# Kernel tuning notes

Measured on AMD Instinct MI355X. Metric: run time of the kernel, lower is better.

## Reference

```python
import jax, jax.numpy as jnp
import numpy as np

B, LAT, MEM, IMG = 8192, 256, 200, 128
THRESHOLD = 1.0 / MEM          # sparse-addressing threshold 1/MEM_DIM
EPS_SHRINK = 1e-12             # module epsilon
EPS_COS = 1e-8                 # torch CosineSimilarity default eps
EPS_L1 = 1e-12                 # torch F.normalize default eps


def setup_inputs() -> dict:
    key = jax.random.key(0)
    k1, k2, k3 = jax.random.split(key, 3)
    z = jax.random.normal(k1, (B, LAT), dtype=jnp.float32)          # encoder latent
    memory = jax.random.normal(k2, (MEM, LAT), dtype=jnp.float32) * 0.05  # kaiming-scale memory
    W = jax.random.normal(k3, (IMG * IMG, LAT), dtype=jnp.float32) * 0.02  # linear weight
    b = jnp.zeros((IMG * IMG,), dtype=jnp.float32)
    return {"z": z, "memory": memory, "W": W, "b": b}


def reference(z, memory, W, b):
    # Cosine similarity via normalized matmul (no [B,MEM,LAT] repeat tensors)
    zn = jnp.linalg.norm(z, axis=1, keepdims=True)          # [B,1]
    mn = jnp.linalg.norm(memory, axis=1, keepdims=True)     # [MEM,1]
    logits = (z @ memory.T) / jnp.maximum(zn * mn.T, EPS_COS)  # [B,MEM]
    w = jax.nn.softmax(logits, axis=1)
    # sparse shrinkage: relu(w-t)*w/(|w-t|+eps)
    w = jax.nn.relu(w - THRESHOLD) * w / (jnp.abs(w - THRESHOLD) + EPS_SHRINK)
    # L1 normalize over memory dim
    w = w / jnp.maximum(jnp.sum(jnp.abs(w), axis=1, keepdims=True), EPS_L1)
    z_hat = w @ memory                                      # [B,LAT]
    x_hat = (z_hat @ W.T + b).reshape(-1, 1, IMG, IMG)      # [B,1,128,128]
    return x_hat, z_hat, w
```

## Files before the change

### kernel.cpp

```cpp
#include <hip/hip_runtime.h>
#include <hip/hip_bf16.h>
#include <stdint.h>

#define B_DIM   8192
#define LAT     256
#define MEM_DIM 200
#define MEM_PAD 208
#define NPIX    16384
#define RPB     16
#define CHUNK   25

typedef short bf16x8 __attribute__((ext_vector_type(8)));
typedef float f32x4  __attribute__((ext_vector_type(4)));

__device__ __forceinline__ float wred_sum(float v) {
#pragma unroll
  for (int m = 32; m; m >>= 1) v += __shfl_xor(v, m, 64);
  return v;
}
__device__ __forceinline__ float wred_max(float v) {
#pragma unroll
  for (int m = 32; m; m >>= 1) v = fmaxf(v, __shfl_xor(v, m, 64));
  return v;
}
__device__ __forceinline__ unsigned short f2bf(float f) {
  unsigned u = __builtin_bit_cast(unsigned, f);
  u = u + 0x7FFFu + ((u >> 16) & 1u);
  return (unsigned short)(u >> 16);
}
__device__ __forceinline__ float bf2f(unsigned short h) {
  return __builtin_bit_cast(float, (unsigned)h << 16);
}
__device__ __forceinline__ void split3(float v, unsigned short& h, unsigned short& m,
                                       unsigned short& l) {
  h = f2bf(v);
  float r1 = v - bf2f(h);
  m = f2bf(r1);
  float r2 = r1 - bf2f(m);
  l = f2bf(r2);
}

__global__ void __launch_bounds__(64) mem_norm_kernel(const float* __restrict__ mem,
                                                      float* __restrict__ mn,
                                                      unsigned short* __restrict__ mem_h,
                                                      unsigned short* __restrict__ mem_m,
                                                      unsigned short* __restrict__ mem_l) {
  const int m = blockIdx.x, lane = threadIdx.x;
  if (m >= MEM_DIM) {
    ushort4 zz = {0, 0, 0, 0};
    ((ushort4*)(mem_h + (size_t)m * LAT))[lane] = zz;
    ((ushort4*)(mem_m + (size_t)m * LAT))[lane] = zz;
    ((ushort4*)(mem_l + (size_t)m * LAT))[lane] = zz;
    return;
  }
  float4 v = ((const float4*)(mem + (size_t)m * LAT))[lane];
  ushort4 h, md, l;
  split3(v.x, h.x, md.x, l.x); split3(v.y, h.y, md.y, l.y);
  split3(v.z, h.z, md.z, l.z); split3(v.w, h.w, md.w, l.w);
  ((ushort4*)(mem_h + (size_t)m * LAT))[lane] = h;
  ((ushort4*)(mem_m + (size_t)m * LAT))[lane] = md;
  ((ushort4*)(mem_l + (size_t)m * LAT))[lane] = l;
  float ss = v.x * v.x + v.y * v.y + v.z * v.z + v.w * v.w;
  ss = wred_sum(ss);
  if (lane == 0) mn[m] = sqrtf(ss);
}

__global__ void __launch_bounds__(256) zsplit_kernel(const float* __restrict__ z,
                                                     unsigned short* __restrict__ z_h,
                                                     unsigned short* __restrict__ z_m,
                                                     unsigned short* __restrict__ z_l) {
  const int i = blockIdx.x * 256 + threadIdx.x;
  float4 v = ((const float4*)z)[i];
  ushort4 h, md, l;
  split3(v.x, h.x, md.x, l.x); split3(v.y, h.y, md.y, l.y);
  split3(v.z, h.z, md.z, l.z); split3(v.w, h.w, md.w, l.w);
  ((ushort4*)z_h)[i] = h;
  ((ushort4*)z_m)[i] = md;
  ((ushort4*)z_l)[i] = l;
}

__global__ void __launch_bounds__(256) convert_w_kernel(const float* __restrict__ W,
                                                        unsigned short* __restrict__ Wb) {
  const int i = blockIdx.x * 256 + threadIdx.x;
  float4 v = ((const float4*)W)[i];
  ushort4 o;
  o.x = f2bf(v.x); o.y = f2bf(v.y); o.z = f2bf(v.z); o.w = f2bf(v.w);
  ((ushort4*)Wb)[i] = o;
}

__global__ void __launch_bounds__(256) row_kernel(
    const float* __restrict__ z, const float* __restrict__ mem,
    const float* __restrict__ mn_g,
    const unsigned short* __restrict__ z_h, const unsigned short* __restrict__ z_m,
    const unsigned short* __restrict__ z_l,
    const unsigned short* __restrict__ mem_h, const unsigned short* __restrict__ mem_m,
    const unsigned short* __restrict__ mem_l,
    float* __restrict__ zhat_out, float* __restrict__ w_out,
    unsigned short* __restrict__ zhat_bf) {
  __shared__ float msh[CHUNK * LAT];
  __shared__ float lw[RPB][MEM_DIM];
  __shared__ float mnsh[MEM_DIM];

  const int tid = threadIdx.x;
  const int lane = tid & 63;
  const int wid = tid >> 6;
  const int row0 = blockIdx.x * RPB;

  if (tid < MEM_DIM) mnsh[tid] = mn_g[tid];

  float4 zr[4];
  float zn[4];
#pragma unroll
  for (int r = 0; r < 4; ++r) {
    const int row = row0 + wid * 4 + r;
    zr[r] = *(const float4*)(z + (size_t)row * LAT + lane * 4);
    float ss = zr[r].x * zr[r].x + zr[r].y * zr[r].y + zr[r].z * zr[r].z + zr[r].w * zr[r].w;
    zn[r] = sqrtf(wred_sum(ss));
  }

  {
    const int fr_ = lane & 15;
    const int kq8 = (lane >> 4) * 8;
    const size_t zoff = (size_t)(row0 + fr_) * LAT + kq8;
    const unsigned short* zh_p = z_h + zoff;
    const unsigned short* zm_p = z_m + zoff;
    const unsigned short* zl_p = z_l + zoff;
    for (int nf = wid; nf <= 12; nf += 4) {
      const size_t moff = (size_t)(nf * 16 + fr_) * LAT + kq8;
      const unsigned short* mh_p = mem_h + moff;
      const unsigned short* mm_p = mem_m + moff;
      const unsigned short* ml_p = mem_l + moff;
      f32x4 a = {};
#pragma unroll
      for (int kk = 0; kk < 8; ++kk) {
        bf16x8 zh = *(const bf16x8*)(zh_p + kk * 32);
        bf16x8 zm = *(const bf16x8*)(zm_p + kk * 32);
        bf16x8 zl = *(const bf16x8*)(zl_p + kk * 32);
        bf16x8 mh = *(const bf16x8*)(mh_p + kk * 32);
        bf16x8 mm = *(const bf16x8*)(mm_p + kk * 32);
        bf16x8 ml = *(const bf16x8*)(ml_p + kk * 32);
        a = __builtin_amdgcn_mfma_f32_16x16x32_bf16(zm, mm, a, 0, 0, 0);
        a = __builtin_amdgcn_mfma_f32_16x16x32_bf16(zh, ml, a, 0, 0, 0);
        a = __builtin_amdgcn_mfma_f32_16x16x32_bf16(zl, mh, a, 0, 0, 0);
        a = __builtin_amdgcn_mfma_f32_16x16x32_bf16(zm, mh, a, 0, 0, 0);
        a = __builtin_amdgcn_mfma_f32_16x16x32_bf16(zh, mm, a, 0, 0, 0);
        a = __builtin_amdgcn_mfma_f32_16x16x32_bf16(zh, mh, a, 0, 0, 0);
      }
      const int m = nf * 16 + fr_;
      if (m < MEM_DIM) {
#pragma unroll
        for (int q = 0; q < 4; ++q)
          lw[(lane >> 4) * 4 + q][m] = a[q];
      }
    }
  }
  __syncthreads();

  const float t = 0.005f;
#pragma unroll
  for (int r = 0; r < 4; ++r) {
    const int lr = wid * 4 + r;
    float lg[4];
#pragma unroll
    for (int i = 0; i < 4; ++i) {
      const int m = lane + 64 * i;
      lg[i] = (m < MEM_DIM) ? lw[lr][m] / fmaxf(zn[r] * mnsh[m], 1e-8f) : -1e30f;
    }
    float mx = wred_max(fmaxf(fmaxf(lg[0], lg[1]), fmaxf(lg[2], lg[3])));
    float e[4]; float s = 0.f;
#pragma unroll
    for (int i = 0; i < 4; ++i) {
      const int m = lane + 64 * i;
      e[i] = (m < MEM_DIM) ? expf(lg[i] - mx) : 0.f;
      s += e[i];
    }
    s = wred_sum(s);
    float sv[4]; float l1 = 0.f;
#pragma unroll
    for (int i = 0; i < 4; ++i) {
      const float wv = e[i] / s;
      const float d = wv - t;
      sv[i] = fmaxf(d, 0.f) * wv / (fabsf(d) + 1e-12f);
      l1 += sv[i];
    }
    l1 = wred_sum(l1);
    const float dnm = fmaxf(l1, 1e-12f);
#pragma unroll
    for (int i = 0; i < 4; ++i) {
      const int m = lane + 64 * i;
      if (m < MEM_DIM) {
        const float wn = sv[i] / dnm;
        lw[lr][m] = wn;
        w_out[(size_t)(row0 + lr) * MEM_DIM + m] = wn;
      }
    }
  }

  f32x4 acc[4] = {};
  for (int c = 0; c < 8; ++c) {
    __syncthreads();
    const float4* gsrc = (const float4*)(mem + (size_t)c * CHUNK * LAT);
    float4* msh4 = (float4*)msh;
    for (int i = tid; i < CHUNK * 64; i += 256) msh4[i] = gsrc[i];
    __syncthreads();
    for (int mm = 0; mm < CHUNK; ++mm) {
      float4 mv = ((float4*)msh)[mm * 64 + lane];
      const int m = c * CHUNK + mm;
#pragma unroll
      for (int r = 0; r < 4; ++r) {
        const float wm = lw[wid * 4 + r][m];
        acc[r][0] += wm * mv.x; acc[r][1] += wm * mv.y;
        acc[r][2] += wm * mv.z; acc[r][3] += wm * mv.w;
      }
    }
  }
#pragma unroll
  for (int r = 0; r < 4; ++r) {
    const int row = row0 + wid * 4 + r;
    float4 o; o.x = acc[r][0]; o.y = acc[r][1]; o.z = acc[r][2]; o.w = acc[r][3];
    *(float4*)(zhat_out + (size_t)row * LAT + lane * 4) = o;
    ushort4 ob; ob.x = f2bf(o.x); ob.y = f2bf(o.y); ob.z = f2bf(o.z); ob.w = f2bf(o.w);
    *(ushort4*)(zhat_bf + (size_t)row * LAT + lane * 4) = ob;
  }
}

#define STAGE(bufbase, t)                                                      \
  {                                                                            \
    const int k0_ = (t) * 32;                                                  \
    _Pragma("unroll")                                                          \
    for (int cc = 0; cc < 2; ++cc) {                                           \
      const int r_ = r0 + cc * 16;                                             \
      __builtin_amdgcn_global_load_lds(                                        \
          (const __attribute__((address_space(1))) void*)(const void*)         \
              (A + (size_t)(brow + r_) * LAT + k0_ + kq),                      \
          (__attribute__((address_space(3))) void*)(void*)                     \
              &smem[(bufbase) + (ch0 + cc) * 1024], 16, 0, 0);                 \
      __builtin_amdgcn_global_load_lds(                                        \
          (const __attribute__((address_space(1))) void*)(const void*)         \
              (Bw + (size_t)(bcol + r_) * LAT + k0_ + kq),                     \
          (__attribute__((address_space(3))) void*)(void*)                     \
              &smem[(bufbase) + 8192 + (ch0 + cc) * 1024], 16, 0, 0);          \
    }                                                                          \
  }

#define GEMM_PROLOG_AND_KLOOP                                                  \
  const int tid = threadIdx.x;                                                 \
  const int lane = tid & 63;                                                   \
  const int wid = tid >> 6;                                                    \
  const int swz = (blockIdx.x & 7) * 1024 + (blockIdx.x >> 3);                 \
  const int st = swz >> 8;                                                     \
  const int loc = swz & 255;                                                   \
  const int tm = (st >> 3) * 16 + (loc & 15);                                  \
  const int tn = (st & 7) * 16 + (loc >> 4);                                   \
  const int brow = tm * 128;                                                   \
  const int bcol = tn * 128;                                                   \
  const int wr = wid >> 1, wc = wid & 1;                                       \
  const int ch0 = wid * 2;                                                     \
  const int r0 = ch0 * 16 + (lane >> 2);                                       \
  const int kq = (lane & 3) * 8;                                               \
  f32x4 acc[4][4] = {};                                                        \
  STAGE(0, 0);                                                                 \
  STAGE(16384, 1);                                                             \
  STAGE(32768, 2);                                                             \
  _Pragma("unroll")                                                            \
  for (int t = 0; t < 8; ++t) {                                                \
    if (t < 6)       asm volatile("s_waitcnt vmcnt(8)" ::: "memory");          \
    else if (t == 6) asm volatile("s_waitcnt vmcnt(4)" ::: "memory");          \
    else             asm volatile("s_waitcnt vmcnt(0)" ::: "memory");          \
    __builtin_amdgcn_sched_barrier(0);                                         \
    __builtin_amdgcn_s_barrier();                                              \
    const int bufb = (t % 3) * 16384;                                          \
    bf16x8 af[4], bfr[4];                                                      \
    _Pragma("unroll")                                                          \
    for (int mf = 0; mf < 4; ++mf)                                             \
      af[mf] = *(const bf16x8*)&smem[bufb + (wr * 64 + mf * 16 + (lane & 15)) * 64 + (lane >> 4) * 16]; \
    _Pragma("unroll")                                                          \
    for (int nf = 0; nf < 4; ++nf)                                             \
      bfr[nf] = *(const bf16x8*)&smem[bufb + 8192 + (wc * 64 + nf * 16 + (lane & 15)) * 64 + (lane >> 4) * 16]; \
    asm volatile("s_waitcnt lgkmcnt(0)" ::: "memory");                         \
    __builtin_amdgcn_sched_barrier(0);                                         \
    __builtin_amdgcn_s_barrier();                                              \
    if (t + 3 < 8) STAGE(((t + 3) % 3) * 16384, t + 3);                        \
    _Pragma("unroll")                                                          \
    for (int mf = 0; mf < 4; ++mf)                                             \
      _Pragma("unroll")                                                        \
      for (int nf = 0; nf < 4; ++nf)                                           \
        acc[mf][nf] = __builtin_amdgcn_mfma_f32_16x16x32_bf16(af[mf], bfr[nf], acc[mf][nf], 0, 0, 0); \
  }

#define TSTRIDE 68
__global__ void __launch_bounds__(256, 3) gemm_xhat_kernel(
    const unsigned short* __restrict__ A, const unsigned short* __restrict__ Bw,
    const float* __restrict__ bias, float* __restrict__ C) {
  __shared__ __align__(16) unsigned char smem[49152];

  if (blockIdx.x < 768) {
    const int d = blockIdx.x >> 8;
    for (int i = 0; i < d; ++i) {
#pragma unroll
      for (int s = 0; s < 8; ++s)
        __builtin_amdgcn_s_sleep(100);
    }
  }

  GEMM_PROLOG_AND_KLOOP

  __syncthreads();
  float* tt = (float*)(smem + wid * (16 * TSTRIDE * 4));

  const int colq = (lane & 15) * 4;
  const int col0 = bcol + wc * 64 + colq;
  const float4 bv4 = *(const float4*)(bias + col0);

#pragma unroll
  for (int mf = 0; mf < 4; ++mf) {
#pragma unroll
    for (int nf = 0; nf < 4; ++nf) {
      const int cl = nf * 16 + (lane & 15);
#pragma unroll
      for (int q = 0; q < 4; ++q)
        tt[((lane >> 4) * 4 + q) * TSTRIDE + cl] = acc[mf][nf][q];
    }
#pragma unroll
    for (int rr = 0; rr < 4; ++rr) {
      const int rl = rr * 4 + (lane >> 4);
      float4 v = *(const float4*)&tt[rl * TSTRIDE + colq];
      f32x4 ve;
      ve[0] = v.x + bv4.x; ve[1] = v.y + bv4.y;
      ve[2] = v.z + bv4.z; ve[3] = v.w + bv4.w;
      const int row = brow + wr * 64 + mf * 16 + rl;
      __builtin_nontemporal_store(ve, (f32x4*)&C[(size_t)row * NPIX + col0]);
    }
  }
}

extern "C" void kernel_launch(void* const* d_in, const int* in_sizes, int n_in,
                              void* d_out, int out_size, void* d_ws, size_t ws_size,
                              hipStream_t stream) {
  const float* z    = (const float*)d_in[0];
  const float* mem  = (const float*)d_in[1];
  const float* W    = (const float*)d_in[2];
  const float* bias = (const float*)d_in[3];

  float* xhat = (float*)d_out;
  float* zhat = xhat + (size_t)B_DIM * NPIX;
  float* wout = zhat + (size_t)B_DIM * LAT;

  unsigned short* z_h   = (unsigned short*)xhat;
  unsigned short* z_m   = z_h + (size_t)B_DIM * LAT;
  unsigned short* z_l   = z_m + (size_t)B_DIM * LAT;
  unsigned short* mem_h = z_l + (size_t)B_DIM * LAT;
  unsigned short* mem_m = mem_h + (size_t)MEM_PAD * LAT;
  unsigned short* mem_l = mem_m + (size_t)MEM_PAD * LAT;

  unsigned short* Wb  = (unsigned short*)d_ws;
  unsigned short* zhb = Wb + (size_t)NPIX * LAT;
  float* mn = (float*)(zhb + (size_t)B_DIM * LAT);

  mem_norm_kernel<<<MEM_PAD, 64, 0, stream>>>(mem, mn, mem_h, mem_m, mem_l);
  zsplit_kernel<<<(B_DIM * LAT / 4) / 256, 256, 0, stream>>>(z, z_h, z_m, z_l);
  convert_w_kernel<<<(NPIX * LAT / 4) / 256, 256, 0, stream>>>(W, Wb);
  row_kernel<<<B_DIM / RPB, 256, 0, stream>>>(z, mem, mn, z_h, z_m, z_l,
                                              mem_h, mem_m, mem_l, zhat, wout, zhb);
  gemm_xhat_kernel<<<8192, 256, 0, stream>>>(zhb, Wb, bias, xhat);
}
```

Baseline: 222.7 us.

## Compute z_hat = w @ memory with split-bf16 MFMA using transposed memory

Replaces the scalar FP32 w@memory loop in row_kernel, which staged memory chunks in LDS, with 3-way bf16-split MFMA products. The memory matrix is pre-transposed and split into high, mid and low bf16 parts in mem_norm_kernel. The weights are split into LDS per block. This aims to move the second small GEMM onto matrix cores while keeping near-FP32 accuracy, at the cost of extra split work, six MFMAs per tile, and more LDS.

```diff
diff --git a/kernel.cpp b/kernel.cpp
--- a/kernel.cpp
+++ b/kernel.cpp
@@ -6,9 +6,10 @@
 #define LAT     256
 #define MEM_DIM 200
 #define MEM_PAD 208
+#define MEMT_K  224
+#define MEMT_S  232
 #define NPIX    16384
 #define RPB     16
-#define CHUNK   25
 
 typedef short bf16x8 __attribute__((ext_vector_type(8)));
 typedef float f32x4  __attribute__((ext_vector_type(4)));
@@ -40,17 +41,25 @@
   l = f2bf(r2);
 }
 
-__global__ void __launch_bounds__(64) mem_norm_kernel(const float* __restrict__ mem,
-                                                      float* __restrict__ mn,
-                                                      unsigned short* __restrict__ mem_h,
-                                                      unsigned short* __restrict__ mem_m,
-                                                      unsigned short* __restrict__ mem_l) {
+__global__ void __launch_bounds__(64) mem_norm_kernel(
+    const float* __restrict__ mem, float* __restrict__ mn,
+    unsigned short* __restrict__ mem_h, unsigned short* __restrict__ mem_m,
+    unsigned short* __restrict__ mem_l,
+    unsigned short* __restrict__ memT_h, unsigned short* __restrict__ memT_m,
+    unsigned short* __restrict__ memT_l) {
   const int m = blockIdx.x, lane = threadIdx.x;
   if (m >= MEM_DIM) {
     ushort4 zz = {0, 0, 0, 0};
-    ((ushort4*)(mem_h + (size_t)m * LAT))[lane] = zz;
-    ((ushort4*)(mem_m + (size_t)m * LAT))[lane] = zz;
-    ((ushort4*)(mem_l + (size_t)m * LAT))[lane] = zz;
+    if (m < MEM_PAD) {
+      ((ushort4*)(mem_h + (size_t)m * LAT))[lane] = zz;
+      ((ushort4*)(mem_m + (size_t)m * LAT))[lane] = zz;
+      ((ushort4*)(mem_l + (size_t)m * LAT))[lane] = zz;
+    }
+#pragma unroll
+    for (int q = 0; q < 4; ++q) {
+      const size_t o = (size_t)(lane * 4 + q) * MEMT_S + m;
+      memT_h[o] = 0; memT_m[o] = 0; memT_l[o] = 0;
+    }
     return;
   }
   float4 v = ((const float4*)(mem + (size_t)m * LAT))[lane];
@@ -60,6 +69,14 @@
   ((ushort4*)(mem_h + (size_t)m * LAT))[lane] = h;
   ((ushort4*)(mem_m + (size_t)m * LAT))[lane] = md;
   ((ushort4*)(mem_l + (size_t)m * LAT))[lane] = l;
+  const float vv[4] = {v.x, v.y, v.z, v.w};
+#pragma unroll
+  for (int q = 0; q < 4; ++q) {
+    unsigned short th, tm, tl;
+    split3(vv[q], th, tm, tl);
+    const size_t o = (size_t)(lane * 4 + q) * MEMT_S + m;
+    memT_h[o] = th; memT_m[o] = tm; memT_l[o] = tl;
+  }
   float ss = v.x * v.x + v.y * v.y + v.z * v.z + v.w * v.w;
   ss = wred_sum(ss);
   if (lane == 0) mn[m] = sqrtf(ss);
@@ -89,38 +106,40 @@
 }
 
 __global__ void __launch_bounds__(256) row_kernel(
-    const float* __restrict__ z, const float* __restrict__ mem,
-    const float* __restrict__ mn_g,
+    const float* __restrict__ z, const float* __restrict__ mn_g,
     const unsigned short* __restrict__ z_h, const unsigned short* __restrict__ z_m,
     const unsigned short* __restrict__ z_l,
     const unsigned short* __restrict__ mem_h, const unsigned short* __restrict__ mem_m,
     const unsigned short* __restrict__ mem_l,
+    const unsigned short* __restrict__ memT_h, const unsigned short* __restrict__ memT_m,
+    const unsigned short* __restrict__ memT_l,
     float* __restrict__ zhat_out, float* __restrict__ w_out,
     unsigned short* __restrict__ zhat_bf) {
-  __shared__ float msh[CHUNK * LAT];
   __shared__ float lw[RPB][MEM_DIM];
   __shared__ float mnsh[MEM_DIM];
+  __shared__ unsigned short whsh[16 * MEMT_S];
+  __shared__ unsigned short wmsh[16 * MEMT_S];
+  __shared__ unsigned short wlsh[16 * MEMT_S];
 
   const int tid = threadIdx.x;
   const int lane = tid & 63;
   const int wid = tid >> 6;
   const int row0 = blockIdx.x * RPB;
+  const int fr_ = lane & 15;
+  const int kq8 = (lane >> 4) * 8;
 
   if (tid < MEM_DIM) mnsh[tid] = mn_g[tid];
 
-  float4 zr[4];
   float zn[4];
 #pragma unroll
   for (int r = 0; r < 4; ++r) {
     const int row = row0 + wid * 4 + r;
-    zr[r] = *(const float4*)(z + (size_t)row * LAT + lane * 4);
-    float ss = zr[r].x * zr[r].x + zr[r].y * zr[r].y + zr[r].z * zr[r].z + zr[r].w * zr[r].w;
+    float4 zr = *(const float4*)(z + (size_t)row * LAT + lane * 4);
+    float ss = zr.x * zr.x + zr.y * zr.y + zr.z * zr.z + zr.w * zr.w;
     zn[r] = sqrtf(wred_sum(ss));
   }
 
   {
-    const int fr_ = lane & 15;
-    const int kq8 = (lane >> 4) * 8;
     const size_t zoff = (size_t)(row0 + fr_) * LAT + kq8;
     const unsigned short* zh_p = z_h + zoff;
     const unsigned short* zm_p = z_m + zoff;
@@ -195,32 +214,49 @@
       }
     }
   }
-
-  f32x4 acc[4] = {};
-  for (int c = 0; c < 8; ++c) {
-    __syncthreads();
-    const float4* gsrc = (const float4*)(mem + (size_t)c * CHUNK * LAT);
-    float4* msh4 = (float4*)msh;
-    for (int i = tid; i < CHUNK * 64; i += 256) msh4[i] = gsrc[i];
-    __syncthreads();
-    for (int mm = 0; mm < CHUNK; ++mm) {
-      float4 mv = ((float4*)msh)[mm * 64 + lane];
-      const int m = c * CHUNK + mm;
-#pragma unroll
-      for (int r = 0; r < 4; ++r) {
-        const float wm = lw[wid * 4 + r][m];
-        acc[r][0] += wm * mv.x; acc[r][1] += wm * mv.y;
-        acc[r][2] += wm * mv.z; acc[r][3] += wm * mv.w;
+  __syncthreads();
+
+  for (int idx = tid; idx < 16 * MEMT_S; idx += 256) {
+    const int lr = idx / MEMT_S, m = idx % MEMT_S;
+    const float val = (m < MEM_DIM) ? lw[lr][m] : 0.f;
+    unsigned short h, md, l;
+    split3(val, h, md, l);
+    whsh[idx] = h; wmsh[idx] = md; wlsh[idx] = l;
+  }
+  __syncthreads();
+
+  {
+    f32x4 zacc[4] = {};
+    for (int kk = 0; kk < 7; ++kk) {
+      const int ko = kk * 32 + kq8;
+      bf16x8 wh = *(const bf16x8*)&whsh[fr_ * MEMT_S + ko];
+      bf16x8 wm = *(const bf16x8*)&wmsh[fr_ * MEMT_S + ko];
+      bf16x8 wl = *(const bf16x8*)&wlsh[fr_ * MEMT_S + ko];
+#pragma unroll
+      for (int nf = 0; nf < 4; ++nf) {
+        const size_t mo = (size_t)(wid * 64 + nf * 16 + fr_) * MEMT_S + ko;
+        bf16x8 th = *(const bf16x8*)(memT_h + mo);
+        bf16x8 tm = *(const bf16x8*)(memT_m + mo);
+        bf16x8 tl = *(const bf16x8*)(memT_l + mo);
+        zacc[nf] = __builtin_amdgcn_mfma_f32_16x16x32_bf16(tm, wm, zacc[nf], 0, 0, 0);
+        zacc[nf] = __builtin_amdgcn_mfma_f32_16x16x32_bf16(th, wl, zacc[nf], 0, 0, 0);
+        zacc[nf] = __builtin_amdgcn_mfma_f32_16x16x32_bf16(tl, wh, zacc[nf], 0, 0, 0);
+        zacc[nf] = __builtin_amdgcn_mfma_f32_16x16x32_bf16(tm, wh, zacc[nf], 0, 0, 0);
+        zacc[nf] = __builtin_amdgcn_mfma_f32_16x16x32_bf16(th, wm, zacc[nf], 0, 0, 0);
+        zacc[nf] = __builtin_amdgcn_mfma_f32_16x16x32_bf16(th, wh, zacc[nf], 0, 0, 0);
       }
     }
-  }
-#pragma unroll
-  for (int r = 0; r < 4; ++r) {
-    const int row = row0 + wid * 4 + r;
-    float4 o; o.x = acc[r][0]; o.y = acc[r][1]; o.z = acc[r][2]; o.w = acc[r][3];
-    *(float4*)(zhat_out + (size_t)row * LAT + lane * 4) = o;
-    ushort4 ob; ob.x = f2bf(o.x); ob.y = f2bf(o.y); ob.z = f2bf(o.z); ob.w = f2bf(o.w);
-    *(ushort4*)(zhat_bf + (size_t)row * LAT + lane * 4) = ob;
+    const size_t orow = (size_t)(row0 + fr_) * LAT;
+#pragma unroll
+    for (int nf = 0; nf < 4; ++nf) {
+      const int d0 = wid * 64 + nf * 16 + (lane >> 4) * 4;
+      float4 o;
+      o.x = zacc[nf][0]; o.y = zacc[nf][1]; o.z = zacc[nf][2]; o.w = zacc[nf][3];
+      *(float4*)(zhat_out + orow + d0) = o;
+      ushort4 ob;
+      ob.x = f2bf(o.x); ob.y = f2bf(o.y); ob.z = f2bf(o.z); ob.w = f2bf(o.w);
+      *(ushort4*)(zhat_bf + orow + d0) = ob;
+    }
   }
 }
 
@@ -346,21 +382,27 @@
   float* zhat = xhat + (size_t)B_DIM * NPIX;
   float* wout = zhat + (size_t)B_DIM * LAT;
 
-  unsigned short* z_h   = (unsigned short*)xhat;
-  unsigned short* z_m   = z_h + (size_t)B_DIM * LAT;
-  unsigned short* z_l   = z_m + (size_t)B_DIM * LAT;
-  unsigned short* mem_h = z_l + (size_t)B_DIM * LAT;
-  unsigned short* mem_m = mem_h + (size_t)MEM_PAD * LAT;
-  unsigned short* mem_l = mem_m + (size_t)MEM_PAD * LAT;
+  unsigned short* z_h    = (unsigned short*)xhat;
+  unsigned short* z_m    = z_h + (size_t)B_DIM * LAT;
+  unsigned short* z_l    = z_m + (size_t)B_DIM * LAT;
+  unsigned short* mem_h  = z_l + (size_t)B_DIM * LAT;
+  unsigned short* mem_m  = mem_h + (size_t)MEM_PAD * LAT;
+  unsigned short* mem_l  = mem_m + (size_t)MEM_PAD * LAT;
+  unsigned short* memT_h = mem_l + (size_t)MEM_PAD * LAT;
+  unsigned short* memT_m = memT_h + (size_t)256 * MEMT_S;
+  unsigned short* memT_l = memT_m + (size_t)256 * MEMT_S;
 
   unsigned short* Wb  = (unsigned short*)d_ws;
   unsigned short* zhb = Wb + (size_t)NPIX * LAT;
   float* mn = (float*)(zhb + (size_t)B_DIM * LAT);
 
-  mem_norm_kernel<<<MEM_PAD, 64, 0, stream>>>(mem, mn, mem_h, mem_m, mem_l);
+  mem_norm_kernel<<<MEMT_K, 64, 0, stream>>>(mem, mn, mem_h, mem_m, mem_l,
+                                             memT_h, memT_m, memT_l);
   zsplit_kernel<<<(B_DIM * LAT / 4) / 256, 256, 0, stream>>>(z, z_h, z_m, z_l);
   convert_w_kernel<<<(NPIX * LAT / 4) / 256, 256, 0, stream>>>(W, Wb);
-  row_kernel<<<B_DIM / RPB, 256, 0, stream>>>(z, mem, mn, z_h, z_m, z_l,
-                                              mem_h, mem_m, mem_l, zhat, wout, zhb);
+  row_kernel<<<B_DIM / RPB, 256, 0, stream>>>(z, mn, z_h, z_m, z_l,
+                                              mem_h, mem_m, mem_l,
+                                              memT_h, memT_m, memT_l,
+                                              zhat, wout, zhb);
   gemm_xhat_kernel<<<8192, 256, 0, stream>>>(zhb, Wb, bias, xhat);
 }
```

After: 217.3 us. 1.03x faster.
